# Kernel optimization log

Measured on AMD Instinct MI355X. Metric: run time of the kernel, lower is better.

Reference implementation:

```python
import jax, jax.numpy as jnp
import numpy as np

N_NODES = 50000
N_EDGES = 800000
D = 128


def gcn_conv(x, W, b, src, dst, num_nodes):
    """PyG GCNConv: x @ W, add self-loops, symmetric normalization, scatter-add, + bias."""
    x = x @ W  # [N, out]
    loop = jnp.arange(num_nodes, dtype=src.dtype)
    s = jnp.concatenate([src, loop])  # [E+N]
    d = jnp.concatenate([dst, loop])
    w = jnp.ones(s.shape[0], x.dtype)  # edge_weight=None -> ones (self-loop fill=1)
    deg = jax.ops.segment_sum(w, d, num_segments=num_nodes)  # [N]
    dinv = jnp.where(deg > 0, jax.lax.rsqrt(deg), 0.0)
    norm = dinv[s] * dinv[d]  # [E+N]
    out = jax.ops.segment_sum(x[s] * norm[:, None], d, num_segments=num_nodes)
    return out + b


def setup_inputs() -> dict:
    key = jax.random.key(0)
    ks = jax.random.split(key, 8)
    sc = 1.0 / np.sqrt(D)
    x = jax.random.normal(ks[0], (N_NODES, D), dtype=jnp.float32)
    edge_index = jax.random.randint(ks[1], (2, N_EDGES), 0, N_NODES)
    W1 = jax.random.normal(ks[2], (D, D), dtype=jnp.float32) * sc
    W2 = jax.random.normal(ks[3], (D, D), dtype=jnp.float32) * sc
    W3 = jax.random.normal(ks[4], (D, D), dtype=jnp.float32) * sc
    b1 = jnp.zeros((D,), jnp.float32)
    b2 = jnp.zeros((D,), jnp.float32)
    b3 = jnp.zeros((D,), jnp.float32)
    return {"x": x, "edge_index": edge_index, "W1": W1, "b1": b1,
            "W2": W2, "b2": b2, "W3": W3, "b3": b3}


def reference(x, edge_index, W1, b1, W2, b2, W3, b3):
    src, dst = edge_index[0], edge_index[1]
    n = x.shape[0]
    x = jax.nn.relu(gcn_conv(x, W1, b1, src, dst, n))
    x = jax.nn.relu(gcn_conv(x, W2, b2, src, dst, n))
    return gcn_conv(x, W3, b3, src, dst, n)
```

## Files before the change

### kernel.cpp

```cpp
#include <hip/hip_runtime.h>
#include <hip/hip_fp16.h>
#include <math.h>

#define D 128

typedef __attribute__((ext_vector_type(8))) _Float16 half8;
typedef __attribute__((ext_vector_type(4))) float f32x4;


__global__ void count_rank_kernel(const int* __restrict__ dst, int* __restrict__ cnt,
                                  int* __restrict__ rank, int E) {
    int e0 = (blockIdx.x * blockDim.x + threadIdx.x) * 8;
    if (e0 + 7 < E) {
        int4 da = *(const int4*)(dst + e0);
        int4 db = *(const int4*)(dst + e0 + 4);
        int4 ra, rb;
        ra.x = atomicAdd(&cnt[da.x], 1);
        ra.y = atomicAdd(&cnt[da.y], 1);
        ra.z = atomicAdd(&cnt[da.z], 1);
        ra.w = atomicAdd(&cnt[da.w], 1);
        rb.x = atomicAdd(&cnt[db.x], 1);
        rb.y = atomicAdd(&cnt[db.y], 1);
        rb.z = atomicAdd(&cnt[db.z], 1);
        rb.w = atomicAdd(&cnt[db.w], 1);
        *(int4*)(rank + e0)     = ra;
        *(int4*)(rank + e0 + 4) = rb;
    } else {
        for (int e = e0; e < E; ++e) rank[e] = atomicAdd(&cnt[dst[e]], 1);
    }
}

__global__ __launch_bounds__(1024) void scan_kernel(const int* __restrict__ cnt,
                                                    int* __restrict__ rowptr,
                                                    float* __restrict__ dinv,
                                                    int N) {
    __shared__ int wsum[16];
    __shared__ int carry_s;
    int tid  = threadIdx.x;
    int lane = tid & 63;
    int wid  = tid >> 6;
    if (tid == 0) carry_s = 0;
    __syncthreads();
    for (int base = 0; base < N; base += 4096) {
        int i = base + tid * 4;
        int4 v = make_int4(0, 0, 0, 0);
        if (i + 3 < N) v = *(const int4*)(cnt + i);
        else {
            if (i + 0 < N) v.x = cnt[i + 0];
            if (i + 1 < N) v.y = cnt[i + 1];
            if (i + 2 < N) v.z = cnt[i + 2];
            if (i + 3 < N) v.w = cnt[i + 3];
        }
        int s0 = v.x, s1 = s0 + v.y, s2 = s1 + v.z, s3 = s2 + v.w;
        int sc = s3;
        #pragma unroll
        for (int off = 1; off < 64; off <<= 1) {
            int t = __shfl_up(sc, off, 64);
            if (lane >= off) sc += t;
        }
        if (lane == 63) wsum[wid] = sc;
        __syncthreads();
        if (tid < 16) {
            int w = wsum[tid];
            #pragma unroll
            for (int off = 1; off < 16; off <<= 1) {
                int t = __shfl_up(w, off, 64);
                if (tid >= off) w += t;
            }
            wsum[tid] = w;
        }
        __syncthreads();
        int waveoff = (wid > 0) ? wsum[wid - 1] : 0;
        int excl = carry_s + waveoff + (sc - s3);
        if (i + 0 < N) { rowptr[i + 0] = excl;      dinv[i + 0] = rsqrtf((float)v.x + 1.0f); }
        if (i + 1 < N) { rowptr[i + 1] = excl + s0; dinv[i + 1] = rsqrtf((float)v.y + 1.0f); }
        if (i + 2 < N) { rowptr[i + 2] = excl + s1; dinv[i + 2] = rsqrtf((float)v.z + 1.0f); }
        if (i + 3 < N) { rowptr[i + 3] = excl + s2; dinv[i + 3] = rsqrtf((float)v.w + 1.0f); }
        __syncthreads();
        if (tid == 0) carry_s += wsum[15];
        __syncthreads();
    }
    if (tid == 0) rowptr[N] = carry_s;
}

__global__ void fill_kernel(const int* __restrict__ src, const int* __restrict__ dst,
                            const int* __restrict__ rank, const int* __restrict__ rowptr,
                            int* __restrict__ col, int E) {
    int e0 = (blockIdx.x * blockDim.x + threadIdx.x) * 8;
    if (e0 + 7 < E) {
        int4 da = *(const int4*)(dst + e0);
        int4 db = *(const int4*)(dst + e0 + 4);
        int4 ra = *(const int4*)(rank + e0);
        int4 rb = *(const int4*)(rank + e0 + 4);
        int4 sa = *(const int4*)(src + e0);
        int4 sb = *(const int4*)(src + e0 + 4);
        int p0 = rowptr[da.x] + ra.x;
        int p1 = rowptr[da.y] + ra.y;
        int p2 = rowptr[da.z] + ra.z;
        int p3 = rowptr[da.w] + ra.w;
        int p4 = rowptr[db.x] + rb.x;
        int p5 = rowptr[db.y] + rb.y;
        int p6 = rowptr[db.z] + rb.z;
        int p7 = rowptr[db.w] + rb.w;
        col[p0] = sa.x; col[p1] = sa.y; col[p2] = sa.z; col[p3] = sa.w;
        col[p4] = sb.x; col[p5] = sb.y; col[p6] = sb.z; col[p7] = sb.w;
    } else {
        for (int e = e0; e < E; ++e) col[rowptr[dst[e]] + rank[e]] = src[e];
    }
}


__global__ void convw_kernel(const float* __restrict__ W1, const float* __restrict__ W2,
                             const float* __restrict__ W3, __half* __restrict__ WhT) {
    int i = blockIdx.x * blockDim.x + threadIdx.x;
    int l = i >> 14;
    int j = i & 16383;
    int n = j >> 7, k = j & 127;
    const float* W = (l == 0) ? W1 : (l == 1) ? W2 : W3;
    WhT[(size_t)i] = __float2half(W[(size_t)k * D + n]);
}


__global__ __launch_bounds__(256) void gemm_mfma_f32(const float* __restrict__ X,
                                                     const __half* __restrict__ WhT,
                                                     const float* __restrict__ dinv,
                                                     __half* __restrict__ Y, int M) {
    int tid  = threadIdx.x;
    int wave = tid >> 6;
    int lane = tid & 63;
    int quad = lane >> 4;
    int l16  = lane & 15;
    int m0   = blockIdx.x * 64 + wave * 16;
    if (m0 >= M) return;

    f32x4 acc[8];
    #pragma unroll
    for (int t = 0; t < 8; ++t) acc[t] = (f32x4)0.0f;

    const float* xrow = X + (size_t)(m0 + l16) * D;

    #pragma unroll
    for (int ks = 0; ks < 4; ++ks) {
        int k0 = ks * 32 + quad * 8;
        float4 x0 = *(const float4*)(xrow + k0);
        float4 x1 = *(const float4*)(xrow + k0 + 4);
        half8 a;
        a[0] = (_Float16)x0.x; a[1] = (_Float16)x0.y;
        a[2] = (_Float16)x0.z; a[3] = (_Float16)x0.w;
        a[4] = (_Float16)x1.x; a[5] = (_Float16)x1.y;
        a[6] = (_Float16)x1.z; a[7] = (_Float16)x1.w;
        #pragma unroll
        for (int t = 0; t < 8; ++t) {
            half8 b = *(const half8*)(WhT + (size_t)(t * 16 + l16) * D + k0);
            acc[t] = __builtin_amdgcn_mfma_f32_16x16x32_f16(a, b, acc[t], 0, 0, 0);
        }
    }

    float4 dv = *(const float4*)(dinv + m0 + quad * 4);
    float dvs[4] = {dv.x, dv.y, dv.z, dv.w};
    #pragma unroll
    for (int t = 0; t < 8; ++t) {
        #pragma unroll
        for (int r = 0; r < 4; ++r) {
            int grow = m0 + quad * 4 + r;
            Y[(size_t)grow * D + t * 16 + l16] = __float2half(acc[t][r] * dvs[r]);
        }
    }
}

__global__ __launch_bounds__(256) void gemm_mfma_f16(const __half* __restrict__ Xh,
                                                     const __half* __restrict__ WhT,
                                                     const float* __restrict__ dinv,
                                                     __half* __restrict__ Y, int M) {
    int tid  = threadIdx.x;
    int wave = tid >> 6;
    int lane = tid & 63;
    int quad = lane >> 4;
    int l16  = lane & 15;
    int m0   = blockIdx.x * 64 + wave * 16;
    if (m0 >= M) return;

    f32x4 acc[8];
    #pragma unroll
    for (int t = 0; t < 8; ++t) acc[t] = (f32x4)0.0f;

    const __half* xrow = Xh + (size_t)(m0 + l16) * D;

    #pragma unroll
    for (int ks = 0; ks < 4; ++ks) {
        int k0 = ks * 32 + quad * 8;
        half8 a = *(const half8*)(xrow + k0);
        #pragma unroll
        for (int t = 0; t < 8; ++t) {
            half8 b = *(const half8*)(WhT + (size_t)(t * 16 + l16) * D + k0);
            acc[t] = __builtin_amdgcn_mfma_f32_16x16x32_f16(a, b, acc[t], 0, 0, 0);
        }
    }

    float4 dv = *(const float4*)(dinv + m0 + quad * 4);
    float dvs[4] = {dv.x, dv.y, dv.z, dv.w};
    #pragma unroll
    for (int t = 0; t < 8; ++t) {
        #pragma unroll
        for (int r = 0; r < 4; ++r) {
            int grow = m0 + quad * 4 + r;
            Y[(size_t)grow * D + t * 16 + l16] = __float2half(acc[t][r] * dvs[r]);
        }
    }
}


#define GATHER(vv, cc) __half2 vv = ((const __half2*)(ys + (size_t)(cc) * D))[lane]

template <bool FINAL>
__global__ __launch_bounds__(256) void aggregate_kernel(const __half* __restrict__ ys,
                                                        const int* __restrict__ rowptr,
                                                        const int* __restrict__ col,
                                                        const float* __restrict__ dinv,
                                                        const float* __restrict__ b,
                                                        __half* __restrict__ outh,
                                                        float* __restrict__ outf,
                                                        int N) {
    int gwave = (blockIdx.x * blockDim.x + threadIdx.x) >> 6;
    int lane  = threadIdx.x & 63;
    if (gwave >= N) return;
    int row = gwave;
    int s = rowptr[row], e = rowptr[row + 1];

    __half2 hself = ((const __half2*)(ys + (size_t)row * D))[lane];
    float2 a0 = __half22float2(hself);
    float2 a1 = make_float2(0.f, 0.f), a2 = make_float2(0.f, 0.f),
           a3 = make_float2(0.f, 0.f), a4 = make_float2(0.f, 0.f),
           a5 = make_float2(0.f, 0.f), a6 = make_float2(0.f, 0.f),
           a7 = make_float2(0.f, 0.f);

    for (int base = s; base < e; base += 64) {
        int idx = base + lane;
        int myc = (idx < e) ? col[idx] : 0;
        int nb  = min(64, e - base);
        int j = 0;
        for (; j + 16 <= nb; j += 16) {
            int c0 = __shfl(myc, j + 0),  c1 = __shfl(myc, j + 1);
            int c2 = __shfl(myc, j + 2),  c3 = __shfl(myc, j + 3);
            int c4 = __shfl(myc, j + 4),  c5 = __shfl(myc, j + 5);
            int c6 = __shfl(myc, j + 6),  c7 = __shfl(myc, j + 7);
            int c8 = __shfl(myc, j + 8),  c9 = __shfl(myc, j + 9);
            int cA = __shfl(myc, j + 10), cB = __shfl(myc, j + 11);
            int cC = __shfl(myc, j + 12), cD = __shfl(myc, j + 13);
            int cE = __shfl(myc, j + 14), cF = __shfl(myc, j + 15);
            GATHER(v0, c0); GATHER(v1, c1); GATHER(v2, c2); GATHER(v3, c3);
            GATHER(v4, c4); GATHER(v5, c5); GATHER(v6, c6); GATHER(v7, c7);
            GATHER(v8, c8); GATHER(v9, c9); GATHER(vA, cA); GATHER(vB, cB);
            GATHER(vC, cC); GATHER(vD, cD); GATHER(vE, cE); GATHER(vF, cF);
            a0.x += __low2float(v0); a0.y += __high2float(v0);
            a1.x += __low2float(v1); a1.y += __high2float(v1);
            a2.x += __low2float(v2); a2.y += __high2float(v2);
            a3.x += __low2float(v3); a3.y += __high2float(v3);
            a4.x += __low2float(v4); a4.y += __high2float(v4);
            a5.x += __low2float(v5); a5.y += __high2float(v5);
            a6.x += __low2float(v6); a6.y += __high2float(v6);
            a7.x += __low2float(v7); a7.y += __high2float(v7);
            a0.x += __low2float(v8); a0.y += __high2float(v8);
            a1.x += __low2float(v9); a1.y += __high2float(v9);
            a2.x += __low2float(vA); a2.y += __high2float(vA);
            a3.x += __low2float(vB); a3.y += __high2float(vB);
            a4.x += __low2float(vC); a4.y += __high2float(vC);
            a5.x += __low2float(vD); a5.y += __high2float(vD);
            a6.x += __low2float(vE); a6.y += __high2float(vE);
            a7.x += __low2float(vF); a7.y += __high2float(vF);
        }
        for (; j + 8 <= nb; j += 8) {
            int c0 = __shfl(myc, j + 0), c1 = __shfl(myc, j + 1);
            int c2 = __shfl(myc, j + 2), c3 = __shfl(myc, j + 3);
            int c4 = __shfl(myc, j + 4), c5 = __shfl(myc, j + 5);
            int c6 = __shfl(myc, j + 6), c7 = __shfl(myc, j + 7);
            GATHER(v0, c0); GATHER(v1, c1); GATHER(v2, c2); GATHER(v3, c3);
            GATHER(v4, c4); GATHER(v5, c5); GATHER(v6, c6); GATHER(v7, c7);
            a0.x += __low2float(v0); a0.y += __high2float(v0);
            a1.x += __low2float(v1); a1.y += __high2float(v1);
            a2.x += __low2float(v2); a2.y += __high2float(v2);
            a3.x += __low2float(v3); a3.y += __high2float(v3);
            a4.x += __low2float(v4); a4.y += __high2float(v4);
            a5.x += __low2float(v5); a5.y += __high2float(v5);
            a6.x += __low2float(v6); a6.y += __high2float(v6);
            a7.x += __low2float(v7); a7.y += __high2float(v7);
        }
        for (; j + 4 <= nb; j += 4) {
            int c0 = __shfl(myc, j + 0), c1 = __shfl(myc, j + 1);
            int c2 = __shfl(myc, j + 2), c3 = __shfl(myc, j + 3);
            GATHER(v0, c0); GATHER(v1, c1); GATHER(v2, c2); GATHER(v3, c3);
            a0.x += __low2float(v0); a0.y += __high2float(v0);
            a1.x += __low2float(v1); a1.y += __high2float(v1);
            a2.x += __low2float(v2); a2.y += __high2float(v2);
            a3.x += __low2float(v3); a3.y += __high2float(v3);
        }
        for (; j < nb; ++j) {
            int c = __shfl(myc, j);
            GATHER(v, c);
            a0.x += __low2float(v); a0.y += __high2float(v);
        }
    }
    a0.x += a1.x + a2.x + a3.x + a4.x + a5.x + a6.x + a7.x;
    a0.y += a1.y + a2.y + a3.y + a4.y + a5.y + a6.y + a7.y;

    float dv  = dinv[row];
    float2 bb = ((const float2*)b)[lane];
    float rx = bb.x + dv * a0.x;
    float ry = bb.y + dv * a0.y;
    if (FINAL) {
        ((float2*)(outf + (size_t)row * D))[lane] = make_float2(rx, ry);
    } else {
        __half2 hv = __floats2half2_rn(fmaxf(rx, 0.f), fmaxf(ry, 0.f));
        ((__half2*)(outh + (size_t)row * D))[lane] = hv;
    }
}


extern "C" void kernel_launch(void* const* d_in, const int* in_sizes, int n_in,
                              void* d_out, int out_size, void* d_ws, size_t ws_size,
                              hipStream_t stream) {
    const float* x   = (const float*)d_in[0];
    const int*   ei  = (const int*)d_in[1];
    const float* W1  = (const float*)d_in[2];
    const float* b1  = (const float*)d_in[3];
    const float* W2  = (const float*)d_in[4];
    const float* b2  = (const float*)d_in[5];
    const float* W3  = (const float*)d_in[6];
    const float* b3  = (const float*)d_in[7];
    float* out = (float*)d_out;

    const int N = in_sizes[0] / D;
    const int E = in_sizes[1] / 2;
    const int* src = ei;
    const int* dst = ei + E;

    char* ws = (char*)d_ws;
    size_t off = 0;
    auto alloc = [&](size_t bytes) {
        void* p = ws + off;
        off = (off + bytes + 255) & ~(size_t)255;
        return p;
    };
    __half* ys    = (__half*)alloc((size_t)N * D * sizeof(__half));
    __half* hs    = (__half*)alloc((size_t)N * D * sizeof(__half));
    int*   cnt    = (int*)alloc((size_t)N * sizeof(int));
    int*   rowptr = (int*)alloc((size_t)(N + 1) * sizeof(int));
    float* dinv   = (float*)alloc((size_t)N * sizeof(float));
    int*   rank   = (int*)alloc((size_t)E * sizeof(int));
    int*   col    = (int*)alloc((size_t)E * sizeof(int));
    __half* WhT   = (__half*)alloc((size_t)3 * D * D * sizeof(__half));
    (void)ws_size; (void)n_in; (void)out_size;

    convw_kernel<<<(3 * D * D + 255) / 256, 256, 0, stream>>>(W1, W2, W3, WhT);

    hipMemsetAsync(cnt, 0, (size_t)N * sizeof(int), stream);
    const int egrid = ((E + 7) / 8 + 255) / 256;
    count_rank_kernel<<<egrid, 256, 0, stream>>>(dst, cnt, rank, E);
    scan_kernel<<<1, 1024, 0, stream>>>(cnt, rowptr, dinv, N);
    fill_kernel<<<egrid, 256, 0, stream>>>(src, dst, rank, rowptr, col, E);

    const int gemm_grid = (N + 63) / 64;
    const int agg_grid  = (N * 64 + 255) / 256;

    gemm_mfma_f32<<<gemm_grid, 256, 0, stream>>>(x, WhT, dinv, ys, N);
    aggregate_kernel<false><<<agg_grid, 256, 0, stream>>>(ys, rowptr, col, dinv, b1, hs, nullptr, N);
    gemm_mfma_f16<<<gemm_grid, 256, 0, stream>>>(hs, WhT + 16384, dinv, ys, N);
    aggregate_kernel<false><<<agg_grid, 256, 0, stream>>>(ys, rowptr, col, dinv, b2, hs, nullptr, N);
    gemm_mfma_f16<<<gemm_grid, 256, 0, stream>>>(hs, WhT + 32768, dinv, ys, N);
    aggregate_kernel<true><<<agg_grid, 256, 0, stream>>>(ys, rowptr, col, dinv, b3, nullptr, out, N);
}
```

Measured before the change: 334.5 us.

## Gather four neighbor rows per wave with 16-byte loads and cross-group reduction

The aggregation kernel now splits each 64-lane wave into four 16-lane groups. Each group loads a whole neighbor row as half8 (16 bytes per lane), so four edges are in flight per step, and the four partial sums are combined with xor shuffles at the end. Padding lanes point at a zero sentinel row appended to ys, which a new memset clears. This aims to cut the number of load instructions and raise bytes per request, at the cost of a shuffle reduction and less unrolled gather parallelism per wave. The fill_kernel edit is only a cosmetic inlining.

Measured after the change: 340.9 us. About the same (+1.9%).

```diff
diff --git a/kernel.cpp b/kernel.cpp
--- a/kernel.cpp
+++ b/kernel.cpp
@@ -94,16 +94,14 @@
         int4 rb = *(const int4*)(rank + e0 + 4);
         int4 sa = *(const int4*)(src + e0);
         int4 sb = *(const int4*)(src + e0 + 4);
-        int p0 = rowptr[da.x] + ra.x;
-        int p1 = rowptr[da.y] + ra.y;
-        int p2 = rowptr[da.z] + ra.z;
-        int p3 = rowptr[da.w] + ra.w;
-        int p4 = rowptr[db.x] + rb.x;
-        int p5 = rowptr[db.y] + rb.y;
-        int p6 = rowptr[db.z] + rb.z;
-        int p7 = rowptr[db.w] + rb.w;
-        col[p0] = sa.x; col[p1] = sa.y; col[p2] = sa.z; col[p3] = sa.w;
-        col[p4] = sb.x; col[p5] = sb.y; col[p6] = sb.z; col[p7] = sb.w;
+        col[rowptr[da.x] + ra.x] = sa.x;
+        col[rowptr[da.y] + ra.y] = sa.y;
+        col[rowptr[da.z] + ra.z] = sa.z;
+        col[rowptr[da.w] + ra.w] = sa.w;
+        col[rowptr[db.x] + rb.x] = sb.x;
+        col[rowptr[db.y] + rb.y] = sb.y;
+        col[rowptr[db.z] + rb.z] = sb.z;
+        col[rowptr[db.w] + rb.w] = sb.w;
     } else {
         for (int e = e0; e < E; ++e) col[rowptr[dst[e]] + rank[e]] = src[e];
     }
@@ -210,7 +208,12 @@
 }
 
 
-#define GATHER(vv, cc) __half2 vv = ((const __half2*)(ys + (size_t)(cc) * D))[lane]
+__device__ __forceinline__ void acc_h8(float2 a[4], half8 v) {
+    a[0].x += (float)v[0]; a[0].y += (float)v[1];
+    a[1].x += (float)v[2]; a[1].y += (float)v[3];
+    a[2].x += (float)v[4]; a[2].y += (float)v[5];
+    a[3].x += (float)v[6]; a[3].y += (float)v[7];
+}
 
 template <bool FINAL>
 __global__ __launch_bounds__(256) void aggregate_kernel(const __half* __restrict__ ys,
@@ -223,95 +226,62 @@
                                                         int N) {
     int gwave = (blockIdx.x * blockDim.x + threadIdx.x) >> 6;
     int lane  = threadIdx.x & 63;
+    int g     = lane >> 4;
+    int l16   = lane & 15;
     if (gwave >= N) return;
     int row = gwave;
     int s = rowptr[row], e = rowptr[row + 1];
 
-    __half2 hself = ((const __half2*)(ys + (size_t)row * D))[lane];
-    float2 a0 = __half22float2(hself);
-    float2 a1 = make_float2(0.f, 0.f), a2 = make_float2(0.f, 0.f),
-           a3 = make_float2(0.f, 0.f), a4 = make_float2(0.f, 0.f),
-           a5 = make_float2(0.f, 0.f), a6 = make_float2(0.f, 0.f),
-           a7 = make_float2(0.f, 0.f);
+    float2 a[4];
+    a[0] = a[1] = a[2] = a[3] = make_float2(0.f, 0.f);
 
     for (int base = s; base < e; base += 64) {
         int idx = base + lane;
-        int myc = (idx < e) ? col[idx] : 0;
+        int myc = (idx < e) ? col[idx] : N;
         int nb  = min(64, e - base);
-        int j = 0;
-        for (; j + 16 <= nb; j += 16) {
-            int c0 = __shfl(myc, j + 0),  c1 = __shfl(myc, j + 1);
-            int c2 = __shfl(myc, j + 2),  c3 = __shfl(myc, j + 3);
-            int c4 = __shfl(myc, j + 4),  c5 = __shfl(myc, j + 5);
-            int c6 = __shfl(myc, j + 6),  c7 = __shfl(myc, j + 7);
-            int c8 = __shfl(myc, j + 8),  c9 = __shfl(myc, j + 9);
-            int cA = __shfl(myc, j + 10), cB = __shfl(myc, j + 11);
-            int cC = __shfl(myc, j + 12), cD = __shfl(myc, j + 13);
-            int cE = __shfl(myc, j + 14), cF = __shfl(myc, j + 15);
-            GATHER(v0, c0); GATHER(v1, c1); GATHER(v2, c2); GATHER(v3, c3);
-            GATHER(v4, c4); GATHER(v5, c5); GATHER(v6, c6); GATHER(v7, c7);
-            GATHER(v8, c8); GATHER(v9, c9); GATHER(vA, cA); GATHER(vB, cB);
-            GATHER(vC, cC); GATHER(vD, cD); GATHER(vE, cE); GATHER(vF, cF);
-            a0.x += __low2float(v0); a0.y += __high2float(v0);
-            a1.x += __low2float(v1); a1.y += __high2float(v1);
-            a2.x += __low2float(v2); a2.y += __high2float(v2);
-            a3.x += __low2float(v3); a3.y += __high2float(v3);
-            a4.x += __low2float(v4); a4.y += __high2float(v4);
-            a5.x += __low2float(v5); a5.y += __high2float(v5);
-            a6.x += __low2float(v6); a6.y += __high2float(v6);
-            a7.x += __low2float(v7); a7.y += __high2float(v7);
-            a0.x += __low2float(v8); a0.y += __high2float(v8);
-            a1.x += __low2float(v9); a1.y += __high2float(v9);
-            a2.x += __low2float(vA); a2.y += __high2float(vA);
-            a3.x += __low2float(vB); a3.y += __high2float(vB);
-            a4.x += __low2float(vC); a4.y += __high2float(vC);
-            a5.x += __low2float(vD); a5.y += __high2float(vD);
-            a6.x += __low2float(vE); a6.y += __high2float(vE);
-            a7.x += __low2float(vF); a7.y += __high2float(vF);
-        }
-        for (; j + 8 <= nb; j += 8) {
-            int c0 = __shfl(myc, j + 0), c1 = __shfl(myc, j + 1);
-            int c2 = __shfl(myc, j + 2), c3 = __shfl(myc, j + 3);
-            int c4 = __shfl(myc, j + 4), c5 = __shfl(myc, j + 5);
-            int c6 = __shfl(myc, j + 6), c7 = __shfl(myc, j + 7);
-            GATHER(v0, c0); GATHER(v1, c1); GATHER(v2, c2); GATHER(v3, c3);
-            GATHER(v4, c4); GATHER(v5, c5); GATHER(v6, c6); GATHER(v7, c7);
-            a0.x += __low2float(v0); a0.y += __high2float(v0);
-            a1.x += __low2float(v1); a1.y += __high2float(v1);
-            a2.x += __low2float(v2); a2.y += __high2float(v2);
-            a3.x += __low2float(v3); a3.y += __high2float(v3);
-            a4.x += __low2float(v4); a4.y += __high2float(v4);
-            a5.x += __low2float(v5); a5.y += __high2float(v5);
-            a6.x += __low2float(v6); a6.y += __high2float(v6);
-            a7.x += __low2float(v7); a7.y += __high2float(v7);
-        }
-        for (; j + 4 <= nb; j += 4) {
-            int c0 = __shfl(myc, j + 0), c1 = __shfl(myc, j + 1);
-            int c2 = __shfl(myc, j + 2), c3 = __shfl(myc, j + 3);
-            GATHER(v0, c0); GATHER(v1, c1); GATHER(v2, c2); GATHER(v3, c3);
-            a0.x += __low2float(v0); a0.y += __high2float(v0);
-            a1.x += __low2float(v1); a1.y += __high2float(v1);
-            a2.x += __low2float(v2); a2.y += __high2float(v2);
-            a3.x += __low2float(v3); a3.y += __high2float(v3);
-        }
-        for (; j < nb; ++j) {
-            int c = __shfl(myc, j);
-            GATHER(v, c);
-            a0.x += __low2float(v); a0.y += __high2float(v);
-        }
-    }
-    a0.x += a1.x + a2.x + a3.x + a4.x + a5.x + a6.x + a7.x;
-    a0.y += a1.y + a2.y + a3.y + a4.y + a5.y + a6.y + a7.y;
-
-    float dv  = dinv[row];
-    float2 bb = ((const float2*)b)[lane];
-    float rx = bb.x + dv * a0.x;
-    float ry = bb.y + dv * a0.y;
+        #pragma unroll 4
+        for (int j = 0; j < nb; j += 4) {
+            int c = __shfl(myc, j + g);
+            half8 v = *(const half8*)(ys + (size_t)c * D + (l16 << 3));
+            acc_h8(a, v);
+        }
+    }
+
+    #pragma unroll
+    for (int k = 0; k < 4; ++k) {
+        a[k].x += __shfl_xor(a[k].x, 16, 64);
+        a[k].y += __shfl_xor(a[k].y, 16, 64);
+        a[k].x += __shfl_xor(a[k].x, 32, 64);
+        a[k].y += __shfl_xor(a[k].y, 32, 64);
+    }
+
+    half8 us = *(const half8*)(ys + (size_t)row * D + (l16 << 3));
+    acc_h8(a, us);
+
+    float dv = dinv[row];
+    float4 b0 = *(const float4*)(b + (l16 << 3));
+    float4 b1 = *(const float4*)(b + (l16 << 3) + 4);
+    float r0 = b0.x + dv * a[0].x, r1 = b0.y + dv * a[0].y;
+    float r2 = b0.z + dv * a[1].x, r3 = b0.w + dv * a[1].y;
+    float r4 = b1.x + dv * a[2].x, r5 = b1.y + dv * a[2].y;
+    float r6 = b1.z + dv * a[3].x, r7 = b1.w + dv * a[3].y;
+
     if (FINAL) {
-        ((float2*)(outf + (size_t)row * D))[lane] = make_float2(rx, ry);
+        if (g == 0)
+            *(float4*)(outf + (size_t)row * D + (l16 << 3)) = make_float4(r0, r1, r2, r3);
+        else if (g == 1)
+            *(float4*)(outf + (size_t)row * D + (l16 << 3) + 4) = make_float4(r4, r5, r6, r7);
     } else {
-        __half2 hv = __floats2half2_rn(fmaxf(rx, 0.f), fmaxf(ry, 0.f));
-        ((__half2*)(outh + (size_t)row * D))[lane] = hv;
+        if (g == 0) {
+            __half2 h0 = __floats2half2_rn(fmaxf(r0, 0.f), fmaxf(r1, 0.f));
+            __half2 h1 = __floats2half2_rn(fmaxf(r2, 0.f), fmaxf(r3, 0.f));
+            __half2 h2 = __floats2half2_rn(fmaxf(r4, 0.f), fmaxf(r5, 0.f));
+            __half2 h3 = __floats2half2_rn(fmaxf(r6, 0.f), fmaxf(r7, 0.f));
+            uint4 pk;
+            pk.x = *(unsigned int*)&h0; pk.y = *(unsigned int*)&h1;
+            pk.z = *(unsigned int*)&h2; pk.w = *(unsigned int*)&h3;
+            *(uint4*)(outh + (size_t)row * D + (l16 << 3)) = pk;
+        }
     }
 }
 
@@ -341,7 +311,7 @@
         off = (off + bytes + 255) & ~(size_t)255;
         return p;
     };
-    __half* ys    = (__half*)alloc((size_t)N * D * sizeof(__half));
+    __half* ys    = (__half*)alloc((size_t)(N + 1) * D * sizeof(__half));
     __half* hs    = (__half*)alloc((size_t)N * D * sizeof(__half));
     int*   cnt    = (int*)alloc((size_t)N * sizeof(int));
     int*   rowptr = (int*)alloc((size_t)(N + 1) * sizeof(int));
@@ -354,6 +324,7 @@
     convw_kernel<<<(3 * D * D + 255) / 256, 256, 0, stream>>>(W1, W2, W3, WhT);
 
     hipMemsetAsync(cnt, 0, (size_t)N * sizeof(int), stream);
+    hipMemsetAsync(ys + (size_t)N * D, 0, (size_t)D * sizeof(__half), stream);
     const int egrid = ((E + 7) / 8 + 255) / 256;
     count_rank_kernel<<<egrid, 256, 0, stream>>>(dst, cnt, rank, E);
     scan_kernel<<<1, 1024, 0, stream>>>(cnt, rowptr, dinv, N);
```
